# Performance work log

Hardware: AMD Instinct MI355X
Metric: run time of the kernel (lower is better)

The kernel has to match this reference:

```python
import jax, jax.numpy as jnp
import numpy as np

B = 512
NODES_PER_GRAPH = 256
N = B * NODES_PER_GRAPH
IN_DIM = 128
HID = 128
PAD_VALUE = -10000.0


def setup_inputs() -> dict:
    key = jax.random.key(0)
    ks = jax.random.split(key, 10)
    inp = {
        "last_node_batch": jax.random.normal(ks[0], (B, IN_DIM), jnp.float32),
        "h": jax.random.normal(ks[1], (N, HID), jnp.float32),
        # NodeEmbed: Linear(in_dim, hidden_dim)
        "W_embed": jax.random.normal(ks[2], (IN_DIM, HID), jnp.float32) / np.sqrt(IN_DIM),
        "b_embed": jnp.zeros((HID,), jnp.float32),
        # Linear_3(2H, 2H, 2)
        "W1": jax.random.normal(ks[3], (2 * HID, 2 * HID), jnp.float32) / np.sqrt(2 * HID),
        "b1": jnp.zeros((2 * HID,), jnp.float32),
        "W2": jax.random.normal(ks[4], (2 * HID, 2 * HID), jnp.float32) / np.sqrt(2 * HID),
        "b2": jnp.zeros((2 * HID,), jnp.float32),
        "W3": jax.random.normal(ks[5], (2 * HID, 2), jnp.float32) / np.sqrt(2 * HID),
        "b3": jnp.zeros((2,), jnp.float32),
        # ragged batch encoded as sorted segment ids (graph id per node)
        "segment_ids": jnp.repeat(jnp.arange(B, dtype=jnp.int64), NODES_PER_GRAPH),
        "max_nodes": NODES_PER_GRAPH,
    }
    return inp


def reference(last_node_batch, h, W_embed, b_embed, W1, b1, W2, b2, W3, b3,
              segment_ids, max_nodes):
    n = h.shape[0]
    b = last_node_batch.shape[0]
    # per-graph node embed, broadcast to each node of its graph (repeat+cat loop)
    node_embed = last_node_batch @ W_embed + b_embed          # [B, H]
    bcast = node_embed[segment_ids]                           # [N, H]
    stack = jnp.concatenate([h, bcast], axis=1)               # [N, 2H]
    # Linear_3 MLP
    out = jnp.tanh(stack @ W1 + b1)
    out = jnp.tanh(out @ W2 + b2)
    edges = out @ W3 + b3                                     # [N, 2]
    # unbatch + pad_sequence(padding_value=-10000), then flatten(1, -1)
    counts = jax.ops.segment_sum(jnp.ones((n,), jnp.int32), segment_ids, num_segments=b)
    offsets = jnp.cumsum(counts) - counts                     # start index of each graph
    pos = jnp.arange(n) - offsets[segment_ids]                # position within graph
    padded = jnp.full((b, max_nodes, 2), PAD_VALUE, dtype=edges.dtype)
    padded = padded.at[segment_ids, pos].set(edges)
    return padded.reshape(b, max_nodes * 2)
```

## Files before the change

kernel.cpp:

```cpp
#include <hip/hip_runtime.h>


typedef __attribute__((ext_vector_type(8))) short s16x8;
typedef __attribute__((ext_vector_type(4))) float f32x4;

#define K2   256
#define KH   128
#define LDK  264

__device__ __forceinline__ float b2f(unsigned short u) {
  return __builtin_bit_cast(float, (unsigned int)u << 16);
}
__device__ __forceinline__ unsigned short f2b(float f) {
  unsigned int u = __builtin_bit_cast(unsigned int, f);
  u += 0x7fffu + ((u >> 16) & 1u);
  return (unsigned short)(u >> 16);
}
__device__ __forceinline__ float pade_tanh(float x) {
  float x2 = x * x;
  float x4 = x2 * x2;
  float num = x * (945.0f + 105.0f * x2 + x4);
  float den = __builtin_fmaf(15.0f, x4, __builtin_fmaf(420.0f, x2, 945.0f));
  float r = num * __builtin_amdgcn_rcpf(den);
  return __builtin_fmaxf(-1.0f, __builtin_fminf(1.0f, r));
}
__device__ __forceinline__ unsigned int probe_is16(const unsigned int* wraw,
                                                   int t) {
  unsigned int w = wraw[t];
  unsigned int e = (w >> 7) & 0xFFu;
  unsigned long long m = __ballot(e >= 96 && e < 128);
  return (__popcll(m) >= 32) ? 1u : 0u;
}

__global__ __launch_bounds__(256) void prep_pack(
    const void* __restrict__ W1, const void* __restrict__ W2,
    const void* __restrict__ Wemb,
    unsigned short* __restrict__ W1P, unsigned short* __restrict__ W2P,
    unsigned short* __restrict__ W1loP)
{
  __shared__ unsigned int flagLds;
  const int blk = blockIdx.x, t = threadIdx.x;
  if (t < 64) { unsigned int f = probe_is16((const unsigned int*)Wemb, t);
                if (t == 0) flagLds = f; }
  __syncthreads();
  const bool is16 = flagLds != 0u;

  const void* S; unsigned short* D; int k0, n0, pk, krow;
  if (blk < 32) { S = W1; D = W1P; pk = 2048; krow = 0;
                  k0 = (blk & 3) * 32; n0 = (blk >> 2) * 32; }
  else if (blk < 96) { int b = blk - 32; S = W2; D = W2P; pk = 4096; krow = 0;
                       k0 = (b & 7) * 32; n0 = (b >> 3) * 32; }
  else { int b = blk - 96; S = W1; D = W1loP; pk = 2048; krow = KH;
         k0 = (b & 3) * 32; n0 = (b >> 2) * 32; }
  #pragma unroll
  for (int q = 0; q < 4; ++q) {
    int idx = t + 256 * q;
    int ln = idx & 31, lk = idx >> 5;
    int n = n0 + ln, k = k0 + lk;
    unsigned short v = is16
        ? ((const unsigned short*)S)[(krow + k) * K2 + n]
        : f2b(((const float*)S)[(krow + k) * K2 + n]);
    D[(n >> 4) * pk + (k >> 3) * 128 + (n & 15) * 8 + (k & 7)] = v;
  }
}

__global__ __launch_bounds__(256, 2) void mlp_graph(
    const void* __restrict__ h,     const void* __restrict__ last,
    const void* __restrict__ Wemb,  const void* __restrict__ bemb,
    const void* __restrict__ b1,    const void* __restrict__ b2,
    const void* __restrict__ W3,    const void* __restrict__ b3,
    const unsigned short* __restrict__ W1P,
    const unsigned short* __restrict__ W2P,
    const unsigned short* __restrict__ W1loP,
    void* __restrict__ out)
{
  __shared__ __align__(16) unsigned short smA[64 * LDK];
  __shared__ float embp[2][KH];
  __shared__ __align__(16) unsigned short embb[KH];
  __shared__ float ebias[K2];
  __shared__ float headp[4][64][2];
  __shared__ unsigned int flagLds;

  const int t    = threadIdx.x;
  const int lane = t & 63, w = t >> 6;
  const int quad = lane >> 4, l16 = lane & 15;
  const int g    = blockIdx.x;

  if (t < 64) { unsigned int f = probe_is16((const unsigned int*)Wemb, t);
                if (t == 0) flagLds = f; }
  __syncthreads();
  const bool is16 = flagLds != 0u;

  {
    const int j = t & 127, half = t >> 7, k0 = half * 64;
    float a0 = 0.f, a1 = 0.f, a2 = 0.f, a3 = 0.f;
    if (is16) {
      const unsigned short* lp = (const unsigned short*)last + g * KH;
      const unsigned short* wp = (const unsigned short*)Wemb;
      #pragma unroll 4
      for (int k = k0; k < k0 + 64; k += 4) {
        a0 += b2f(lp[k])     * b2f(wp[k * KH + j]);
        a1 += b2f(lp[k + 1]) * b2f(wp[(k + 1) * KH + j]);
        a2 += b2f(lp[k + 2]) * b2f(wp[(k + 2) * KH + j]);
        a3 += b2f(lp[k + 3]) * b2f(wp[(k + 3) * KH + j]);
      }
    } else {
      const float* lp = (const float*)last + g * KH;
      const float* wp = (const float*)Wemb;
      #pragma unroll 4
      for (int k = k0; k < k0 + 64; k += 4) {
        a0 += lp[k]     * wp[k * KH + j];
        a1 += lp[k + 1] * wp[(k + 1) * KH + j];
        a2 += lp[k + 2] * wp[(k + 2) * KH + j];
        a3 += lp[k + 3] * wp[(k + 3) * KH + j];
      }
    }
    embp[half][j] = (a0 + a1) + (a2 + a3);
  }

  s16x8 w1f[16];
  #pragma unroll
  for (int kk = 0; kk < 4; ++kk)
    #pragma unroll
    for (int c = 0; c < 4; ++c)
      w1f[kk * 4 + c] = *(const s16x8*)&W1P[(w * 4 + c) * 2048
                                            + (kk * 4 + quad) * 128 + l16 * 8];
  s16x8 bh[2];
  #pragma unroll
  for (int s = 0; s < 2; ++s) {
    int kk = 2 * w + s;
    #pragma unroll
    for (int j = 0; j < 8; ++j) {
      int kidx = (kk * 32 + quad * 8 + j) * 2 + (l16 & 1);
      bh[s][j] = is16 ? (short)((const unsigned short*)W3)[kidx]
                      : (short)f2b(((const float*)W3)[kidx]);
    }
  }
  float b2v[4];
  #pragma unroll
  for (int c = 0; c < 4; ++c) {
    int col = w * 64 + c * 16 + l16;
    b2v[c] = is16 ? b2f(((const unsigned short*)b2)[col])
                  : ((const float*)b2)[col];
  }
  float b3e = 0.f;
  if (t < 128)
    b3e = is16 ? b2f(((const unsigned short*)b3)[t & 1])
               : ((const float*)b3)[t & 1];
  __syncthreads();

  if (t < KH) {
    float e = is16 ? b2f(((const unsigned short*)bemb)[t])
                   : ((const float*)bemb)[t];
    embb[t] = f2b(e + embp[0][t] + embp[1][t]);
  }
  __syncthreads();

  {
    f32x4 eacc[4];
    #pragma unroll
    for (int c = 0; c < 4; ++c) eacc[c] = f32x4{0.f, 0.f, 0.f, 0.f};
    #pragma unroll
    for (int kk = 0; kk < 4; ++kk) {
      s16x8 a = *(const s16x8*)&embb[kk * 32 + quad * 8];
      #pragma unroll
      for (int c = 0; c < 4; ++c) {
        s16x8 b = *(const s16x8*)&W1loP[(w * 4 + c) * 2048
                                        + (kk * 4 + quad) * 128 + l16 * 8];
        eacc[c] = __builtin_amdgcn_mfma_f32_16x16x32_bf16(a, b, eacc[c],
                                                          0, 0, 0);
      }
    }
    if (quad == 0) {
      #pragma unroll
      for (int c = 0; c < 4; ++c) {
        int col = w * 64 + c * 16 + l16;
        float bb = is16 ? b2f(((const unsigned short*)b1)[col])
                        : ((const float*)b1)[col];
        ebias[col] = bb + eacc[c][0];
      }
    }
  }

  uint4 hreg[4];
  const int pr = t >> 4, pc = t & 15;
  auto load_tile = [&](int tile) {
    int rbase = g * 256 + tile * 64;
    if (is16) {
      const uint4* hp = (const uint4*)h;
      #pragma unroll
      for (int i = 0; i < 4; ++i)
        hreg[i] = hp[(size_t)(rbase + pr + 16 * i) * 16 + pc];
    } else {
      const float4* hf = (const float4*)h;
      #pragma unroll
      for (int i = 0; i < 4; ++i) {
        float4 va = hf[(size_t)(rbase + pr + 16 * i) * 32 + pc * 2];
        float4 vb = hf[(size_t)(rbase + pr + 16 * i) * 32 + pc * 2 + 1];
        ushort4 ua, ub;
        ua.x = f2b(va.x); ua.y = f2b(va.y); ua.z = f2b(va.z); ua.w = f2b(va.w);
        ub.x = f2b(vb.x); ub.y = f2b(vb.y); ub.z = f2b(vb.z); ub.w = f2b(vb.w);
        hreg[i] = make_uint4(
            (unsigned)ua.x | ((unsigned)ua.y << 16),
            (unsigned)ua.z | ((unsigned)ua.w << 16),
            (unsigned)ub.x | ((unsigned)ub.y << 16),
            (unsigned)ub.z | ((unsigned)ub.w << 16));
      }
    }
  };
  load_tile(0);

  f32x4 acc[4][4];
  for (int tile = 0; tile < 4; ++tile) {
    const int base = g * 256 + tile * 64;
    __syncthreads();
    #pragma unroll
    for (int i = 0; i < 4; ++i)
      *(uint4*)&smA[(pr + 16 * i) * LDK + pc * 8] = hreg[i];
    if (tile < 3) load_tile(tile + 1);
    __syncthreads();

    #pragma unroll
    for (int i = 0; i < 4; ++i)
      #pragma unroll
      for (int c = 0; c < 4; ++c) acc[i][c] = f32x4{0.f, 0.f, 0.f, 0.f};
    #pragma unroll
    for (int kk = 0; kk < 4; ++kk) {
      s16x8 a[4];
      #pragma unroll
      for (int i = 0; i < 4; ++i)
        a[i] = *(const s16x8*)&smA[(i * 16 + l16) * LDK + kk * 32 + quad * 8];
      #pragma unroll
      for (int i = 0; i < 4; ++i)
        #pragma unroll
        for (int c = 0; c < 4; ++c)
          acc[i][c] = __builtin_amdgcn_mfma_f32_16x16x32_bf16(
              a[i], w1f[kk * 4 + c], acc[i][c], 0, 0, 0);
    }
    __syncthreads();
    #pragma unroll
    for (int c = 0; c < 4; ++c) {
      int col = w * 64 + c * 16 + l16;
      float eb = ebias[col];
      #pragma unroll
      for (int i = 0; i < 4; ++i)
        #pragma unroll
        for (int rg = 0; rg < 4; ++rg)
          smA[(i * 16 + quad * 4 + rg) * LDK + col] =
              f2b(pade_tanh(acc[i][c][rg] + eb));
    }
    __syncthreads();

    #pragma unroll
    for (int i = 0; i < 4; ++i)
      #pragma unroll
      for (int c = 0; c < 4; ++c) acc[i][c] = f32x4{0.f, 0.f, 0.f, 0.f};
    #pragma unroll 2
    for (int kk = 0; kk < 8; ++kk) {
      s16x8 a[4], b[4];
      #pragma unroll
      for (int i = 0; i < 4; ++i)
        a[i] = *(const s16x8*)&smA[(i * 16 + l16) * LDK + kk * 32 + quad * 8];
      #pragma unroll
      for (int c = 0; c < 4; ++c)
        b[c] = *(const s16x8*)&W2P[(w * 4 + c) * 4096
                                   + (kk * 4 + quad) * 128 + l16 * 8];
      #pragma unroll
      for (int i = 0; i < 4; ++i)
        #pragma unroll
        for (int c = 0; c < 4; ++c)
          acc[i][c] = __builtin_amdgcn_mfma_f32_16x16x32_bf16(
              a[i], b[c], acc[i][c], 0, 0, 0);
    }
    __syncthreads();
    #pragma unroll
    for (int c = 0; c < 4; ++c) {
      int col = w * 64 + c * 16 + l16;
      #pragma unroll
      for (int i = 0; i < 4; ++i)
        #pragma unroll
        for (int rg = 0; rg < 4; ++rg)
          smA[(i * 16 + quad * 4 + rg) * LDK + col] =
              f2b(pade_tanh(acc[i][c][rg] + b2v[c]));
    }
    __syncthreads();

    {
      f32x4 accH[4];
      #pragma unroll
      for (int i = 0; i < 4; ++i) accH[i] = f32x4{0.f, 0.f, 0.f, 0.f};
      #pragma unroll
      for (int s = 0; s < 2; ++s) {
        int kk = 2 * w + s;
        #pragma unroll
        for (int i = 0; i < 4; ++i) {
          s16x8 a = *(const s16x8*)&smA[(i * 16 + l16) * LDK
                                        + kk * 32 + quad * 8];
          accH[i] = __builtin_amdgcn_mfma_f32_16x16x32_bf16(
              a, bh[s], accH[i], 0, 0, 0);
        }
      }
      if (l16 < 2) {
        #pragma unroll
        for (int i = 0; i < 4; ++i)
          #pragma unroll
          for (int rg = 0; rg < 4; ++rg)
            headp[w][i * 16 + quad * 4 + rg][l16] = accH[i][rg];
      }
    }
    __syncthreads();
    if (t < 128) {
      const int r = t >> 1, e = t & 1;
      float s = b3e + headp[0][r][e] + headp[1][r][e]
                    + headp[2][r][e] + headp[3][r][e];
      size_t idx = (size_t)(base + r) * 2 + e;
      if (is16) ((unsigned short*)out)[idx] = f2b(s);
      else      ((float*)out)[idx] = s;
    }
  }
}

extern "C" void kernel_launch(void* const* d_in, const int* in_sizes, int n_in,
                              void* d_out, int out_size, void* d_ws, size_t ws_size,
                              hipStream_t stream) {
  (void)in_sizes; (void)n_in; (void)out_size; (void)ws_size;
  const void* last = d_in[0];
  const void* h    = d_in[1];
  const void* Wemb = d_in[2];
  const void* bemb = d_in[3];
  const void* W1   = d_in[4];
  const void* b1   = d_in[5];
  const void* W2   = d_in[6];
  const void* b2   = d_in[7];
  const void* W3   = d_in[8];
  const void* b3   = d_in[9];

  char* ws = (char*)d_ws;
  unsigned short* W1P   = (unsigned short*)(ws);
  unsigned short* W2P   = (unsigned short*)(ws + 65536);
  unsigned short* W1loP = (unsigned short*)(ws + 196608);

  prep_pack<<<dim3(128), dim3(256), 0, stream>>>(W1, W2, Wemb, W1P, W2P, W1loP);
  mlp_graph<<<dim3(512), dim3(256), 0, stream>>>(
      h, last, Wemb, bemb, b1, b2, W3, b3, W1P, W2P, W1loP, d_out);
}
```

Measured before the change: 161.0 us.

## Split each graph across two blocks and transpose MFMA operand roles

Doubles the grid so each block handles 128 nodes of a graph instead of 256, and raises the occupancy hint to 3 blocks per CU. The MFMA operands are swapped so weights become the A operand and node activations the B operand. This lets the bias be held in registers and the tanh outputs be written as packed 64-bit stores. The output head becomes one MFMA chain per wave with W3 staged in LDS, which removes the cross-wave head reduction and one barrier. The node-embed prologue and W1 low-half MFMA are now repeated per half-graph, and W1 fragments are reloaded from global memory every k-step instead of being kept in registers.

```diff
diff --git a/kernel.cpp b/kernel.cpp
--- a/kernel.cpp
+++ b/kernel.cpp
@@ -15,6 +15,9 @@
   unsigned int u = __builtin_bit_cast(unsigned int, f);
   u += 0x7fffu + ((u >> 16) & 1u);
   return (unsigned short)(u >> 16);
+}
+__device__ __forceinline__ unsigned int pk2(float a, float b) {
+  return (unsigned int)f2b(a) | ((unsigned int)f2b(b) << 16);
 }
 __device__ __forceinline__ float pade_tanh(float x) {
   float x2 = x * x;
@@ -64,7 +67,7 @@
   }
 }
 
-__global__ __launch_bounds__(256, 2) void mlp_graph(
+__global__ __launch_bounds__(256, 3) void mlp_graph(
     const void* __restrict__ h,     const void* __restrict__ last,
     const void* __restrict__ Wemb,  const void* __restrict__ bemb,
     const void* __restrict__ b1,    const void* __restrict__ b2,
@@ -77,22 +80,45 @@
   __shared__ __align__(16) unsigned short smA[64 * LDK];
   __shared__ float embp[2][KH];
   __shared__ __align__(16) unsigned short embb[KH];
-  __shared__ float ebias[K2];
-  __shared__ float headp[4][64][2];
+  __shared__ __align__(16) unsigned short w3lds[3][K2];
   __shared__ unsigned int flagLds;
 
   const int t    = threadIdx.x;
   const int lane = t & 63, w = t >> 6;
   const int quad = lane >> 4, l16 = lane & 15;
-  const int g    = blockIdx.x;
+  const int gb   = blockIdx.x;
+  const int g    = gb >> 1;
+  const int row0 = g * 256 + (gb & 1) * 128;
 
   if (t < 64) { unsigned int f = probe_is16((const unsigned int*)Wemb, t);
                 if (t == 0) flagLds = f; }
   __syncthreads();
   const bool is16 = flagLds != 0u;
 
+  uint4 hreg[4];
+  const int pr = t >> 4, pc = t & 15;
+  auto load_tile = [&](int tile) {
+    int rbase = row0 + tile * 64;
+    if (is16) {
+      const uint4* hp = (const uint4*)h;
+      #pragma unroll
+      for (int i = 0; i < 4; ++i)
+        hreg[i] = hp[(size_t)(rbase + pr + 16 * i) * 16 + pc];
+    } else {
+      const float4* hf = (const float4*)h;
+      #pragma unroll
+      for (int i = 0; i < 4; ++i) {
+        float4 va = hf[(size_t)(rbase + pr + 16 * i) * 32 + pc * 2];
+        float4 vb = hf[(size_t)(rbase + pr + 16 * i) * 32 + pc * 2 + 1];
+        hreg[i] = make_uint4(pk2(va.x, va.y), pk2(va.z, va.w),
+                             pk2(vb.x, vb.y), pk2(vb.z, vb.w));
+      }
+    }
+  };
+  load_tile(0);
+
   {
-    const int j = t & 127, half = t >> 7, k0 = half * 64;
+    const int j = t & 127, kh2 = t >> 7, k0 = kh2 * 64;
     float a0 = 0.f, a1 = 0.f, a2 = 0.f, a3 = 0.f;
     if (is16) {
       const unsigned short* lp = (const unsigned short*)last + g * KH;
@@ -115,38 +141,16 @@
         a3 += lp[k + 3] * wp[(k + 3) * KH + j];
       }
     }
-    embp[half][j] = (a0 + a1) + (a2 + a3);
-  }
-
-  s16x8 w1f[16];
-  #pragma unroll
-  for (int kk = 0; kk < 4; ++kk)
-    #pragma unroll
-    for (int c = 0; c < 4; ++c)
-      w1f[kk * 4 + c] = *(const s16x8*)&W1P[(w * 4 + c) * 2048
-                                            + (kk * 4 + quad) * 128 + l16 * 8];
-  s16x8 bh[2];
-  #pragma unroll
-  for (int s = 0; s < 2; ++s) {
-    int kk = 2 * w + s;
-    #pragma unroll
-    for (int j = 0; j < 8; ++j) {
-      int kidx = (kk * 32 + quad * 8 + j) * 2 + (l16 & 1);
-      bh[s][j] = is16 ? (short)((const unsigned short*)W3)[kidx]
-                      : (short)f2b(((const float*)W3)[kidx]);
-    }
-  }
-  float b2v[4];
-  #pragma unroll
-  for (int c = 0; c < 4; ++c) {
-    int col = w * 64 + c * 16 + l16;
-    b2v[c] = is16 ? b2f(((const unsigned short*)b2)[col])
-                  : ((const float*)b2)[col];
-  }
-  float b3e = 0.f;
-  if (t < 128)
-    b3e = is16 ? b2f(((const unsigned short*)b3)[t & 1])
-               : ((const float*)b3)[t & 1];
+    embp[kh2][j] = (a0 + a1) + (a2 + a3);
+  }
+  for (int s = t; s < 2 * K2; s += 256) {
+    int e = s & 1, k = s >> 1;
+    w3lds[e][k] = is16 ? ((const unsigned short*)W3)[k * 2 + e]
+                       : f2b(((const float*)W3)[k * 2 + e]);
+  }
+  w3lds[2][t] = 0;
+  float b30 = is16 ? b2f(((const unsigned short*)b3)[0]) : ((const float*)b3)[0];
+  float b31 = is16 ? b2f(((const unsigned short*)b3)[1]) : ((const float*)b3)[1];
   __syncthreads();
 
   if (t < KH) {
@@ -156,99 +160,84 @@
   }
   __syncthreads();
 
+  float ebv[4][4];
   {
     f32x4 eacc[4];
     #pragma unroll
-    for (int c = 0; c < 4; ++c) eacc[c] = f32x4{0.f, 0.f, 0.f, 0.f};
+    for (int i = 0; i < 4; ++i) eacc[i] = f32x4{0.f, 0.f, 0.f, 0.f};
     #pragma unroll
     for (int kk = 0; kk < 4; ++kk) {
-      s16x8 a = *(const s16x8*)&embb[kk * 32 + quad * 8];
-      #pragma unroll
-      for (int c = 0; c < 4; ++c) {
-        s16x8 b = *(const s16x8*)&W1loP[(w * 4 + c) * 2048
+      s16x8 be = *(const s16x8*)&embb[kk * 32 + quad * 8];
+      #pragma unroll
+      for (int i = 0; i < 4; ++i) {
+        s16x8 a = *(const s16x8*)&W1loP[(w * 4 + i) * 2048
                                         + (kk * 4 + quad) * 128 + l16 * 8];
-        eacc[c] = __builtin_amdgcn_mfma_f32_16x16x32_bf16(a, b, eacc[c],
+        eacc[i] = __builtin_amdgcn_mfma_f32_16x16x32_bf16(a, be, eacc[i],
                                                           0, 0, 0);
       }
     }
-    if (quad == 0) {
-      #pragma unroll
-      for (int c = 0; c < 4; ++c) {
-        int col = w * 64 + c * 16 + l16;
-        float bb = is16 ? b2f(((const unsigned short*)b1)[col])
-                        : ((const float*)b1)[col];
-        ebias[col] = bb + eacc[c][0];
-      }
-    }
-  }
-
-  uint4 hreg[4];
-  const int pr = t >> 4, pc = t & 15;
-  auto load_tile = [&](int tile) {
-    int rbase = g * 256 + tile * 64;
-    if (is16) {
-      const uint4* hp = (const uint4*)h;
-      #pragma unroll
-      for (int i = 0; i < 4; ++i)
-        hreg[i] = hp[(size_t)(rbase + pr + 16 * i) * 16 + pc];
-    } else {
-      const float4* hf = (const float4*)h;
+    #pragma unroll
+    for (int i = 0; i < 4; ++i)
+      #pragma unroll
+      for (int rg = 0; rg < 4; ++rg) {
+        int f = (w * 4 + i) * 16 + quad * 4 + rg;
+        float bb = is16 ? b2f(((const unsigned short*)b1)[f])
+                        : ((const float*)b1)[f];
+        ebv[i][rg] = bb + eacc[i][rg];
+      }
+  }
+  float b2v[4][4];
+  #pragma unroll
+  for (int i = 0; i < 4; ++i)
+    #pragma unroll
+    for (int rg = 0; rg < 4; ++rg) {
+      int f = (w * 4 + i) * 16 + quad * 4 + rg;
+      b2v[i][rg] = is16 ? b2f(((const unsigned short*)b2)[f])
+                        : ((const float*)b2)[f];
+    }
+
+  f32x4 acc[4][4];
+  for (int tile = 0; tile < 2; ++tile) {
+    const int base = row0 + tile * 64;
+    __syncthreads();
+    #pragma unroll
+    for (int i = 0; i < 4; ++i)
+      *(uint4*)&smA[(pr + 16 * i) * LDK + pc * 8] = hreg[i];
+    if (tile == 0) load_tile(1);
+    __syncthreads();
+
+    #pragma unroll
+    for (int i = 0; i < 4; ++i)
+      #pragma unroll
+      for (int c = 0; c < 4; ++c) acc[i][c] = f32x4{0.f, 0.f, 0.f, 0.f};
+    #pragma unroll
+    for (int kk = 0; kk < 4; ++kk) {
+      s16x8 bf[4];
+      #pragma unroll
+      for (int c = 0; c < 4; ++c)
+        bf[c] = *(const s16x8*)&smA[(c * 16 + l16) * LDK + kk * 32 + quad * 8];
       #pragma unroll
       for (int i = 0; i < 4; ++i) {
-        float4 va = hf[(size_t)(rbase + pr + 16 * i) * 32 + pc * 2];
-        float4 vb = hf[(size_t)(rbase + pr + 16 * i) * 32 + pc * 2 + 1];
-        ushort4 ua, ub;
-        ua.x = f2b(va.x); ua.y = f2b(va.y); ua.z = f2b(va.z); ua.w = f2b(va.w);
-        ub.x = f2b(vb.x); ub.y = f2b(vb.y); ub.z = f2b(vb.z); ub.w = f2b(vb.w);
-        hreg[i] = make_uint4(
-            (unsigned)ua.x | ((unsigned)ua.y << 16),
-            (unsigned)ua.z | ((unsigned)ua.w << 16),
-            (unsigned)ub.x | ((unsigned)ub.y << 16),
-            (unsigned)ub.z | ((unsigned)ub.w << 16));
-      }
-    }
-  };
-  load_tile(0);
-
-  f32x4 acc[4][4];
-  for (int tile = 0; tile < 4; ++tile) {
-    const int base = g * 256 + tile * 64;
-    __syncthreads();
-    #pragma unroll
-    for (int i = 0; i < 4; ++i)
-      *(uint4*)&smA[(pr + 16 * i) * LDK + pc * 8] = hreg[i];
-    if (tile < 3) load_tile(tile + 1);
-    __syncthreads();
-
-    #pragma unroll
-    for (int i = 0; i < 4; ++i)
-      #pragma unroll
-      for (int c = 0; c < 4; ++c) acc[i][c] = f32x4{0.f, 0.f, 0.f, 0.f};
-    #pragma unroll
-    for (int kk = 0; kk < 4; ++kk) {
-      s16x8 a[4];
-      #pragma unroll
-      for (int i = 0; i < 4; ++i)
-        a[i] = *(const s16x8*)&smA[(i * 16 + l16) * LDK + kk * 32 + quad * 8];
-      #pragma unroll
-      for (int i = 0; i < 4; ++i)
+        s16x8 a = *(const s16x8*)&W1P[(w * 4 + i) * 2048
+                                      + (kk * 4 + quad) * 128 + l16 * 8];
         #pragma unroll
         for (int c = 0; c < 4; ++c)
           acc[i][c] = __builtin_amdgcn_mfma_f32_16x16x32_bf16(
-              a[i], w1f[kk * 4 + c], acc[i][c], 0, 0, 0);
-    }
-    __syncthreads();
-    #pragma unroll
-    for (int c = 0; c < 4; ++c) {
-      int col = w * 64 + c * 16 + l16;
-      float eb = ebias[col];
-      #pragma unroll
-      for (int i = 0; i < 4; ++i)
-        #pragma unroll
-        for (int rg = 0; rg < 4; ++rg)
-          smA[(i * 16 + quad * 4 + rg) * LDK + col] =
-              f2b(pade_tanh(acc[i][c][rg] + eb));
-    }
+              a, bf[c], acc[i][c], 0, 0, 0);
+      }
+    }
+    __syncthreads();
+    #pragma unroll
+    for (int i = 0; i < 4; ++i)
+      #pragma unroll
+      for (int c = 0; c < 4; ++c) {
+        uint2 d;
+        d.x = pk2(pade_tanh(acc[i][c][0] + ebv[i][0]),
+                  pade_tanh(acc[i][c][1] + ebv[i][1]));
+        d.y = pk2(pade_tanh(acc[i][c][2] + ebv[i][2]),
+                  pade_tanh(acc[i][c][3] + ebv[i][3]));
+        *(uint2*)&smA[(c * 16 + l16) * LDK + (w * 4 + i) * 16 + quad * 4] = d;
+      }
     __syncthreads();
 
     #pragma unroll
@@ -257,65 +246,50 @@
       for (int c = 0; c < 4; ++c) acc[i][c] = f32x4{0.f, 0.f, 0.f, 0.f};
     #pragma unroll 2
     for (int kk = 0; kk < 8; ++kk) {
-      s16x8 a[4], b[4];
-      #pragma unroll
-      for (int i = 0; i < 4; ++i)
-        a[i] = *(const s16x8*)&smA[(i * 16 + l16) * LDK + kk * 32 + quad * 8];
+      s16x8 bf[4];
       #pragma unroll
       for (int c = 0; c < 4; ++c)
-        b[c] = *(const s16x8*)&W2P[(w * 4 + c) * 4096
-                                   + (kk * 4 + quad) * 128 + l16 * 8];
-      #pragma unroll
-      for (int i = 0; i < 4; ++i)
+        bf[c] = *(const s16x8*)&smA[(c * 16 + l16) * LDK + kk * 32 + quad * 8];
+      #pragma unroll
+      for (int i = 0; i < 4; ++i) {
+        s16x8 a = *(const s16x8*)&W2P[(w * 4 + i) * 4096
+                                      + (kk * 4 + quad) * 128 + l16 * 8];
         #pragma unroll
         for (int c = 0; c < 4; ++c)
           acc[i][c] = __builtin_amdgcn_mfma_f32_16x16x32_bf16(
-              a[i], b[c], acc[i][c], 0, 0, 0);
-    }
-    __syncthreads();
-    #pragma unroll
-    for (int c = 0; c < 4; ++c) {
-      int col = w * 64 + c * 16 + l16;
-      #pragma unroll
-      for (int i = 0; i < 4; ++i)
-        #pragma unroll
-        for (int rg = 0; rg < 4; ++rg)
-          smA[(i * 16 + quad * 4 + rg) * LDK + col] =
-              f2b(pade_tanh(acc[i][c][rg] + b2v[c]));
-    }
+              a, bf[c], acc[i][c], 0, 0, 0);
+      }
+    }
+    __syncthreads();
+    #pragma unroll
+    for (int i = 0; i < 4; ++i)
+      #pragma unroll
+      for (int c = 0; c < 4; ++c) {
+        uint2 d;
+        d.x = pk2(pade_tanh(acc[i][c][0] + b2v[i][0]),
+                  pade_tanh(acc[i][c][1] + b2v[i][1]));
+        d.y = pk2(pade_tanh(acc[i][c][2] + b2v[i][2]),
+                  pade_tanh(acc[i][c][3] + b2v[i][3]));
+        *(uint2*)&smA[(c * 16 + l16) * LDK + (w * 4 + i) * 16 + quad * 4] = d;
+      }
     __syncthreads();
 
     {
-      f32x4 accH[4];
-      #pragma unroll
-      for (int i = 0; i < 4; ++i) accH[i] = f32x4{0.f, 0.f, 0.f, 0.f};
-      #pragma unroll
-      for (int s = 0; s < 2; ++s) {
-        int kk = 2 * w + s;
-        #pragma unroll
-        for (int i = 0; i < 4; ++i) {
-          s16x8 a = *(const s16x8*)&smA[(i * 16 + l16) * LDK
-                                        + kk * 32 + quad * 8];
-          accH[i] = __builtin_amdgcn_mfma_f32_16x16x32_bf16(
-              a, bh[s], accH[i], 0, 0, 0);
-        }
-      }
-      if (l16 < 2) {
-        #pragma unroll
-        for (int i = 0; i < 4; ++i)
-          #pragma unroll
-          for (int rg = 0; rg < 4; ++rg)
-            headp[w][i * 16 + quad * 4 + rg][l16] = accH[i][rg];
-      }
-    }
-    __syncthreads();
-    if (t < 128) {
-      const int r = t >> 1, e = t & 1;
-      float s = b3e + headp[0][r][e] + headp[1][r][e]
-                    + headp[2][r][e] + headp[3][r][e];
-      size_t idx = (size_t)(base + r) * 2 + e;
-      if (is16) ((unsigned short*)out)[idx] = f2b(s);
-      else      ((float*)out)[idx] = s;
+      f32x4 hacc = f32x4{0.f, 0.f, 0.f, 0.f};
+      const unsigned short* w3row = w3lds[l16 < 2 ? l16 : 2];
+      #pragma unroll
+      for (int kk = 0; kk < 8; ++kk) {
+        s16x8 a3 = *(const s16x8*)&w3row[kk * 32 + quad * 8];
+        s16x8 bf = *(const s16x8*)&smA[(w * 16 + l16) * LDK
+                                       + kk * 32 + quad * 8];
+        hacc = __builtin_amdgcn_mfma_f32_16x16x32_bf16(a3, bf, hacc, 0, 0, 0);
+      }
+      if (quad == 0) {
+        int node = base + w * 16 + l16;
+        float e0 = hacc[0] + b30, e1 = hacc[1] + b31;
+        if (is16) ((unsigned int*)out)[node] = pk2(e0, e1);
+        else *(float2*)((float*)out + (size_t)node * 2) = make_float2(e0, e1);
+      }
     }
   }
 }
@@ -341,6 +315,6 @@
   unsigned short* W1loP = (unsigned short*)(ws + 196608);
 
   prep_pack<<<dim3(128), dim3(256), 0, stream>>>(W1, W2, Wemb, W1P, W2P, W1loP);
-  mlp_graph<<<dim3(512), dim3(256), 0, stream>>>(
+  mlp_graph<<<dim3(1024), dim3(256), 0, stream>>>(
       h, last, Wemb, bemb, b1, b2, W3, b3, W1P, W2P, W1loP, d_out);
 }
```

New measurement: 218.6 us. +35.8%, slower.
